# Performance work log

Measured on AMD Instinct MI355X. Metric: run time of the kernel, lower is better.

## Reference

```python
import jax, jax.numpy as jnp
import numpy as np

NUM_HEADS = 16
STRIDE = 32
WINDOW = 64  # local window half-width hard-coded in the original forward


def setup_inputs() -> dict:
    key = jax.random.key(0)
    k0, k1, k2 = jax.random.split(key, 3)
    d = 1024
    return {
        "x": jax.random.normal(k0, (1, 2048, d), dtype=jnp.float32),
        "w_qkv": jax.random.normal(k1, (d, 3 * d), dtype=jnp.float32) / np.sqrt(d),
        "b_qkv": jnp.zeros((3 * d,), dtype=jnp.float32),
        "w_out": jax.random.normal(k2, (d, d), dtype=jnp.float32) / np.sqrt(d),
        "b_out": jnp.zeros((d,), dtype=jnp.float32),
    }


def _sparse_mask(n: int) -> jnp.ndarray:
    # mask[i, j] True if j is a strided column (j % stride == 0)
    # or j is within the +/-WINDOW local band of i.
    i = jnp.arange(n)[:, None]
    j = jnp.arange(n)[None, :]
    return (j % STRIDE == 0) | (jnp.abs(i - j) <= WINDOW)


def reference(x, w_qkv, b_qkv, w_out, b_out):
    b, n, d = x.shape
    h = NUM_HEADS
    dh = d // h
    scale = dh ** (-0.5)

    qkv = x @ w_qkv + b_qkv  # [b, n, 3d]
    q, k, v = jnp.split(qkv, 3, axis=-1)
    q = q.reshape(b, n, h, dh).transpose(0, 2, 1, 3)  # [b, h, n, dh]
    k = k.reshape(b, n, h, dh).transpose(0, 2, 1, 3)
    v = v.reshape(b, n, h, dh).transpose(0, 2, 1, 3)

    scores = jnp.einsum("bhid,bhjd->bhij", q, k) * scale  # [b, h, n, n]
    mask = _sparse_mask(n)  # [n, n], broadcast over b, h
    scores = jnp.where(mask, scores, -jnp.inf)
    attn = jax.nn.softmax(scores, axis=-1)

    out = jnp.einsum("bhij,bhjd->bhid", attn, v)  # [b, h, n, dh]
    out = out.transpose(0, 2, 1, 3).reshape(b, n, d)
    return out @ w_out + b_out
```

## Files before the change

kernel.cpp:

```cpp
#include <hip/hip_runtime.h>

typedef unsigned short u16;
typedef __attribute__((ext_vector_type(8))) short bf16x8;
typedef __attribute__((ext_vector_type(4))) float f32x4;

__device__ __forceinline__ u16 f2bf(float f) {
  union { float f; unsigned u; } v; v.f = f;
  unsigned u = v.u;
  return (u16)((u + 0x7FFFu + ((u >> 16) & 1u)) >> 16);
}

__device__ __forceinline__ void gld16(const void* g, void* l) {
  __builtin_amdgcn_global_load_lds((const __attribute__((address_space(1))) void*)g,
                                   (__attribute__((address_space(3))) void*)l, 16, 0, 0);
}

__device__ __forceinline__ void tconv64(const float* __restrict__ in, u16* __restrict__ out,
                                        int R, int C, int bc, int br, float* t) {
  const int tid = threadIdx.x;
  const int c0 = bc * 64, r0 = br * 64;
  const int hi = tid >> 4, lo = tid & 15;
#pragma unroll
  for (int it = 0; it < 4; ++it) {
    int r = it * 16 + hi;
    float4 f = *(const float4*)&in[(size_t)(r0 + r) * C + c0 + lo * 4];
    float* tr = &t[r * 65 + lo * 4];
    tr[0] = f.x; tr[1] = f.y; tr[2] = f.z; tr[3] = f.w;
  }
  __syncthreads();
#pragma unroll
  for (int it = 0; it < 4; ++it) {
    int cc = it * 16 + hi;
    ushort4 o;
    o.x = f2bf(t[(lo * 4 + 0) * 65 + cc]);
    o.y = f2bf(t[(lo * 4 + 1) * 65 + cc]);
    o.z = f2bf(t[(lo * 4 + 2) * 65 + cc]);
    o.w = f2bf(t[(lo * 4 + 3) * 65 + cc]);
    *(ushort4*)&out[(size_t)(c0 + cc) * R + r0 + lo * 4] = o;
  }
}

__global__ __launch_bounds__(256) void prep(const float* __restrict__ x, u16* __restrict__ xb,
                                            const float* __restrict__ wq, u16* __restrict__ wqT,
                                            const float* __restrict__ wo, u16* __restrict__ woT) {
  __shared__ float t[64 * 65];
  int b = blockIdx.x;
  if (b < 1024) {
    int i = (b * 256 + threadIdx.x) * 8;
    float4 f0 = *(const float4*)(x + i);
    float4 f1 = *(const float4*)(x + i + 4);
    ushort4 r0, r1;
    r0.x = f2bf(f0.x); r0.y = f2bf(f0.y); r0.z = f2bf(f0.z); r0.w = f2bf(f0.w);
    r1.x = f2bf(f1.x); r1.y = f2bf(f1.y); r1.z = f2bf(f1.z); r1.w = f2bf(f1.w);
    *(ushort4*)(xb + i) = r0;
    *(ushort4*)(xb + i + 4) = r1;
  } else if (b < 1024 + 768) {
    int b2 = b - 1024;
    tconv64(wq, wqT, 1024, 3072, b2 % 48, b2 / 48, t);
  } else {
    int b3 = b - 1792;
    tconv64(wo, woT, 1024, 1024, b3 & 15, b3 >> 4, t);
  }
}

#define GEMM_STAGE(As, Bs, A, BT, buf, kt, BM, BN, MT, NT)                        \
  {                                                                               \
    _Pragma("unroll")                                                             \
    for (int it = 0; it < MT; ++it) {                                             \
      int G = wv * (MT * 64) + it * 64 + lane;                                    \
      int r = G >> 3, g = G & 7, gs = g ^ (r & 7);                                \
      gld16(&A[(size_t)(m0 + r) * K + (kt) + gs * 8],                             \
            &As[buf][(wv * (MT * 64) + it * 64) * 8]);                            \
    }                                                                             \
    _Pragma("unroll")                                                             \
    for (int it = 0; it < NT; ++it) {                                             \
      int G = wv * (NT * 64) + it * 64 + lane;                                    \
      int r = G >> 3, g = G & 7, gs = g ^ (r & 7);                                \
      gld16(&BT[(size_t)(n0 + r) * K + (kt) + gs * 8],                            \
            &Bs[buf][(wv * (NT * 64) + it * 64) * 8]);                            \
    }                                                                             \
  }

#define GEMM_COMPUTE(As, Bs, buf, BM, BN, MT, NT)                                 \
  {                                                                               \
    _Pragma("unroll")                                                             \
    for (int ks = 0; ks < 2; ++ks) {                                              \
      bf16x8 av[MT], bv[NT];                                                      \
      _Pragma("unroll")                                                           \
      for (int m = 0; m < MT; ++m) {                                              \
        int r = wm * (BM / 2) + m * 16 + lr;                                      \
        av[m] = *(const bf16x8*)&As[buf][r * 64 + (((ks * 4 + lg) ^ (r & 7)) * 8)]; \
      }                                                                           \
      _Pragma("unroll")                                                           \
      for (int n = 0; n < NT; ++n) {                                              \
        int r = wn * (BN / 2) + n * 16 + lr;                                      \
        bv[n] = *(const bf16x8*)&Bs[buf][r * 64 + (((ks * 4 + lg) ^ (r & 7)) * 8)]; \
      }                                                                           \
      _Pragma("unroll")                                                           \
      for (int m = 0; m < MT; ++m)                                                \
        _Pragma("unroll")                                                         \
        for (int n = 0; n < NT; ++n)                                              \
          acc[m][n] = __builtin_amdgcn_mfma_f32_16x16x32_bf16(av[m], bv[n],       \
                                                              acc[m][n], 0, 0, 0); \
    }                                                                             \
  }

__global__ __launch_bounds__(256) void gemm_qkv(const u16* __restrict__ A,
                                                const u16* __restrict__ BT,
                                                const float* __restrict__ bias,
                                                u16* __restrict__ qkv3,
                                                u16* __restrict__ vT,
                                                u16* __restrict__ vTs,
                                                int K) {
  constexpr int BM = 128, BN = 64, MT = 4, NT = 2;
  __shared__ u16 As[2][BM * 64];
  __shared__ u16 Bs[2][BN * 64];
  const int tid = threadIdx.x;
  const int lane = tid & 63, wv = tid >> 6;
  const int lr = lane & 15, lg = lane >> 4;
  const int wm = wv >> 1, wn = wv & 1;
  const int m0 = blockIdx.y * BM, n0 = blockIdx.x * BN;

  f32x4 acc[MT][NT] = {};

  GEMM_STAGE(As, Bs, A, BT, 0, 0, BM, BN, MT, NT);
  __syncthreads();
  int cur = 0;
  for (int kt = 64; kt < K; kt += 64) {
    GEMM_STAGE(As, Bs, A, BT, cur ^ 1, kt, BM, BN, MT, NT);
    GEMM_COMPUTE(As, Bs, cur, BM, BN, MT, NT);
    __syncthreads();
    cur ^= 1;
  }
  GEMM_COMPUTE(As, Bs, cur, BM, BN, MT, NT);

  if (n0 < 2048) {
#pragma unroll
    for (int m = 0; m < MT; ++m)
#pragma unroll
      for (int n = 0; n < NT; ++n) {
        int col = n0 + wn * 32 + n * 16 + lr;
        float bcol = bias[col];
#pragma unroll
        for (int qq = 0; qq < 4; ++qq) {
          int row = m0 + wm * 64 + m * 16 + 4 * lg + qq;
          qkv3[(size_t)row * 3072 + col] = f2bf(acc[m][n][qq] + bcol);
        }
      }
  } else {
    __syncthreads();
    u16* T = &As[0][0];
#pragma unroll
    for (int m = 0; m < MT; ++m)
#pragma unroll
      for (int n = 0; n < NT; ++n) {
        int col = wn * 32 + n * 16 + lr;
        float bcol = bias[n0 + col];
#pragma unroll
        for (int qq = 0; qq < 4; ++qq) {
          int row = wm * 64 + m * 16 + 4 * lg + qq;
          T[col * 132 + row] = f2bf(acc[m][n][qq] + bcol);
        }
      }
    __syncthreads();
    const int dgb = n0 - 2048;
#pragma unroll
    for (int c = wv; c < 64; c += 4) {
      uint val = (uint)T[c * 132 + lane * 2] | ((uint)T[c * 132 + lane * 2 + 1] << 16);
      *(uint*)&vT[(size_t)(dgb + c) * 2048 + m0 + lane * 2] = val;
    }
    {
      int rr = tid >> 6, c = tid & 63;
      vTs[(size_t)(dgb + c) * 64 + (m0 >> 5) + rr] = T[c * 132 + rr * 32];
    }
  }
}

__global__ __launch_bounds__(256) void gemm_out(const u16* __restrict__ A,
                                                const u16* __restrict__ BT,
                                                const float* __restrict__ bias,
                                                float* __restrict__ Cp,
                                                int K) {
  constexpr int BM = 64, BN = 64, MT = 2, NT = 2;
  __shared__ u16 As[2][BM * 64];
  __shared__ u16 Bs[2][BN * 64];
  const int tid = threadIdx.x;
  const int lane = tid & 63, wv = tid >> 6;
  const int lr = lane & 15, lg = lane >> 4;
  const int wm = wv >> 1, wn = wv & 1;
  const int m0 = blockIdx.y * BM, n0 = blockIdx.x * BN;

  f32x4 acc[MT][NT] = {};

  GEMM_STAGE(As, Bs, A, BT, 0, 0, BM, BN, MT, NT);
  __syncthreads();
  int cur = 0;
  for (int kt = 64; kt < K; kt += 64) {
    GEMM_STAGE(As, Bs, A, BT, cur ^ 1, kt, BM, BN, MT, NT);
    GEMM_COMPUTE(As, Bs, cur, BM, BN, MT, NT);
    __syncthreads();
    cur ^= 1;
  }
  GEMM_COMPUTE(As, Bs, cur, BM, BN, MT, NT);

#pragma unroll
  for (int m = 0; m < MT; ++m)
#pragma unroll
    for (int n = 0; n < NT; ++n) {
      int col = n0 + wn * 32 + n * 16 + lr;
      float bcol = bias[col];
#pragma unroll
      for (int qq = 0; qq < 4; ++qq) {
        int row = m0 + wm * 32 + m * 16 + 4 * lg + qq;
        Cp[(size_t)row * 1024 + col] = acc[m][n][qq] + bcol;
      }
    }
}

__global__ __launch_bounds__(64) void sattn(const u16* __restrict__ qkv,
                                            const u16* __restrict__ vT,
                                            const u16* __restrict__ vTs,
                                            u16* __restrict__ ao) {
  const int h = blockIdx.x;
  const int i0 = blockIdx.y * 16;
  const int ws = i0 - 64;
  const int lane = threadIdx.x;
  const int lr = lane & 15, lg = lane >> 4;

  __shared__ __attribute__((aligned(16))) u16 Ps[16][232];

  const u16* qp = &qkv[(size_t)(i0 + lr) * 3072 + h * 64 + lg * 8];
  bf16x8 qa0 = *(const bf16x8*)qp;
  bf16x8 qa1 = *(const bf16x8*)(qp + 32);

  const u16* kp[13];
#pragma unroll
  for (int n = 0; n < 13; ++n) {
    int col = n * 16 + lr;
    int j = (col < 144) ? (ws + col) : ((col - 144) << 5);
    j = j < 0 ? 0 : (j > 2047 ? 2047 : j);
    kp[n] = &qkv[(size_t)j * 3072 + 1024 + h * 64 + lg * 8];
  }

  f32x4 sc[13];
#pragma unroll
  for (int n = 0; n < 13; ++n) {
    bf16x8 k0 = *(const bf16x8*)kp[n];
    bf16x8 k1 = *(const bf16x8*)(kp[n] + 32);
    f32x4 a = {0.f, 0.f, 0.f, 0.f};
    a = __builtin_amdgcn_mfma_f32_16x16x32_bf16(qa0, k0, a, 0, 0, 0);
    a = __builtin_amdgcn_mfma_f32_16x16x32_bf16(qa1, k1, a, 0, 0, 0);
    sc[n] = a;
  }

  float mx[4] = {-1e30f, -1e30f, -1e30f, -1e30f};
#pragma unroll
  for (int n = 0; n < 13; ++n) {
    int col = n * 16 + lr;
    int jw = ws + col;
    int js = (col - 144) << 5;
    bool isw = col < 144;
#pragma unroll
    for (int qq = 0; qq < 4; ++qq) {
      int i = i0 + 4 * lg + qq;
      bool ok;
      if (isw) {
        int dd = i - jw; dd = dd < 0 ? -dd : dd;
        ok = (jw >= 0) && (jw < 2048) && ((dd <= 64) || ((jw & 31) == 0));
      } else {
        ok = (js < ws) || (js > ws + 143);
      }
      float v = ok ? sc[n][qq] * 0.125f : -1e30f;
      sc[n][qq] = v;
      mx[qq] = fmaxf(mx[qq], v);
    }
  }
#pragma unroll
  for (int qq = 0; qq < 4; ++qq) {
    float v = mx[qq];
    v = fmaxf(v, __shfl_xor(v, 1));
    v = fmaxf(v, __shfl_xor(v, 2));
    v = fmaxf(v, __shfl_xor(v, 4));
    v = fmaxf(v, __shfl_xor(v, 8));
    mx[qq] = v;
  }

  float sm[4] = {0.f, 0.f, 0.f, 0.f};
#pragma unroll
  for (int n = 0; n < 13; ++n) {
#pragma unroll
    for (int qq = 0; qq < 4; ++qq) {
      float p = __expf(sc[n][qq] - mx[qq]);
      sm[qq] += p;
      Ps[4 * lg + qq][n * 16 + lr] = f2bf(p);
    }
  }
#pragma unroll
  for (int qq = 0; qq < 4; ++qq) {
    float s = sm[qq];
    s += __shfl_xor(s, 1);
    s += __shfl_xor(s, 2);
    s += __shfl_xor(s, 4);
    s += __shfl_xor(s, 8);
    sm[qq] = s;
  }
  {
    ushort4 z; z.x = 0; z.y = 0; z.z = 0; z.w = 0;
    *(ushort4*)&Ps[lane >> 2][208 + (lane & 3) * 4] = z;
  }
  __syncthreads();

  f32x4 ov[4] = {{0.f,0.f,0.f,0.f},{0.f,0.f,0.f,0.f},{0.f,0.f,0.f,0.f},{0.f,0.f,0.f,0.f}};
#pragma unroll
  for (int ksb = 0; ksb < 7; ++ksb) {
    bf16x8 pa = *(const bf16x8*)&Ps[lr][ksb * 32 + lg * 8];
    int c0 = ksb * 32 + lg * 8;
#pragma unroll
    for (int n = 0; n < 4; ++n) {
      int d = n * 16 + lr;
      const u16* vp;
      if (c0 < 144) {
        int jb = ws + c0;
        jb = jb < 0 ? 0 : (jb > 2040 ? 2040 : jb);
        vp = &vT[(size_t)(h * 64 + d) * 2048 + jb];
      } else if (c0 < 208) {
        vp = &vTs[((size_t)(h * 64 + d) << 6) + (c0 - 144)];
      } else {
        vp = &vTs[(size_t)(h * 64 + d) << 6];
      }
      bf16x8 vb = *(const bf16x8*)vp;
      ov[n] = __builtin_amdgcn_mfma_f32_16x16x32_bf16(pa, vb, ov[n], 0, 0, 0);
    }
  }

#pragma unroll
  for (int qq = 0; qq < 4; ++qq) {
    float inv = 1.0f / sm[qq];
    int row = i0 + 4 * lg + qq;
#pragma unroll
    for (int n = 0; n < 4; ++n)
      ao[(size_t)row * 1024 + h * 64 + n * 16 + lr] = f2bf(ov[n][qq] * inv);
  }
}

extern "C" void kernel_launch(void* const* d_in, const int* in_sizes, int n_in,
                              void* d_out, int out_size, void* d_ws, size_t ws_size,
                              hipStream_t stream) {
  (void)in_sizes; (void)n_in; (void)out_size; (void)ws_size;
  const float* x     = (const float*)d_in[0];
  const float* w_qkv = (const float*)d_in[1];
  const float* b_qkv = (const float*)d_in[2];
  const float* w_out = (const float*)d_in[3];
  const float* b_out = (const float*)d_in[4];
  float* out = (float*)d_out;
  char* ws = (char*)d_ws;

  u16* xb    = (u16*)(ws);
  u16* wqkvT = (u16*)(ws + 4194304);
  u16* woutT = (u16*)(ws + 10485760);
  u16* qkv3  = (u16*)(ws + 12582912);
  u16* attnb = (u16*)(ws + 25165824);
  u16* vT    = (u16*)(ws + 29360128);
  u16* vTs   = (u16*)(ws + 33554432);

  prep<<<2048, 256, 0, stream>>>(x, xb, w_qkv, wqkvT, w_out, woutT);
  gemm_qkv<<<dim3(3072 / 64, 2048 / 128), 256, 0, stream>>>(xb, wqkvT, b_qkv, qkv3, vT, vTs,
                                                            1024);
  sattn<<<dim3(16, 128), 64, 0, stream>>>(qkv3, vT, vTs, attnb);
  gemm_out<<<dim3(1024 / 64, 2048 / 64), 256, 0, stream>>>(attnb, woutT, b_out, out, 1024);
}
```

Baseline: 63.14 us.

## Stage shared K/V tiles in LDS across four query waves per attention block

The sparse attention kernel now processes 64 query rows per block with four waves. Each block loads a 192-column window of K plus 64 strided columns, and the matching V^T slice, into swizzled LDS using direct global-to-LDS loads, so the waves share them instead of each wave fetching K/V from global memory on its own. The window widens from 144 to 192 columns, which adds masked MFMA work, and the larger LDS footprint may reduce occupancy.

```diff
diff --git a/kernel.cpp b/kernel.cpp
--- a/kernel.cpp
+++ b/kernel.cpp
@@ -217,36 +217,59 @@
     }
 }
 
-__global__ __launch_bounds__(64) void sattn(const u16* __restrict__ qkv,
-                                            const u16* __restrict__ vT,
-                                            const u16* __restrict__ vTs,
-                                            u16* __restrict__ ao) {
+__global__ __launch_bounds__(256) void sattn(const u16* __restrict__ qkv,
+                                             const u16* __restrict__ vT,
+                                             const u16* __restrict__ vTs,
+                                             u16* __restrict__ ao) {
   const int h = blockIdx.x;
-  const int i0 = blockIdx.y * 16;
-  const int ws = i0 - 64;
-  const int lane = threadIdx.x;
+  const int i0b = blockIdx.y * 64;
+  const int ws = i0b - 64;
+  const int tid = threadIdx.x;
+  const int lane = tid & 63, wv = tid >> 6;
   const int lr = lane & 15, lg = lane >> 4;
 
-  __shared__ __attribute__((aligned(16))) u16 Ps[16][232];
-
+  __shared__ __attribute__((aligned(16))) u16 Kl[256 * 64];
+  __shared__ __attribute__((aligned(16))) u16 Vl[64 * 256];
+  __shared__ __attribute__((aligned(16))) u16 Ps[4][16][264];
+
+#pragma unroll
+  for (int it = 0; it < 8; ++it) {
+    {
+      int ck = wv * 8 + it;
+      int c = 8 * ck + (lane >> 3);
+      int g = lane & 7, gs = g ^ (c & 7);
+      int j = (c < 192) ? (ws + c) : ((c - 192) << 5);
+      j = j < 0 ? 0 : (j > 2047 ? 2047 : j);
+      gld16(&qkv[(size_t)j * 3072 + 1024 + h * 64 + gs * 8], &Kl[ck * 512]);
+    }
+    {
+      int tv = wv * 8 + it;
+      int d = 2 * tv + (lane >> 5);
+      int g = lane & 31, gs = g ^ (d & 7);
+      const u16* src;
+      if (gs < 24) {
+        int c0 = ws + gs * 8;
+        c0 = c0 < 0 ? 0 : (c0 > 2040 ? 2040 : c0);
+        src = &vT[(size_t)(h * 64 + d) * 2048 + c0];
+      } else {
+        src = &vTs[(size_t)(h * 64 + d) * 64 + (gs - 24) * 8];
+      }
+      gld16(src, &Vl[tv * 512]);
+    }
+  }
+  __syncthreads();
+
+  const int i0 = i0b + wv * 16;
   const u16* qp = &qkv[(size_t)(i0 + lr) * 3072 + h * 64 + lg * 8];
   bf16x8 qa0 = *(const bf16x8*)qp;
   bf16x8 qa1 = *(const bf16x8*)(qp + 32);
 
-  const u16* kp[13];
-#pragma unroll
-  for (int n = 0; n < 13; ++n) {
-    int col = n * 16 + lr;
-    int j = (col < 144) ? (ws + col) : ((col - 144) << 5);
-    j = j < 0 ? 0 : (j > 2047 ? 2047 : j);
-    kp[n] = &qkv[(size_t)j * 3072 + 1024 + h * 64 + lg * 8];
-  }
-
-  f32x4 sc[13];
-#pragma unroll
-  for (int n = 0; n < 13; ++n) {
-    bf16x8 k0 = *(const bf16x8*)kp[n];
-    bf16x8 k1 = *(const bf16x8*)(kp[n] + 32);
+  f32x4 sc[16];
+#pragma unroll
+  for (int n = 0; n < 16; ++n) {
+    int c = n * 16 + lr;
+    bf16x8 k0 = *(const bf16x8*)&Kl[c * 64 + ((lg ^ (c & 7)) * 8)];
+    bf16x8 k1 = *(const bf16x8*)&Kl[c * 64 + (((4 + lg) ^ (c & 7)) * 8)];
     f32x4 a = {0.f, 0.f, 0.f, 0.f};
     a = __builtin_amdgcn_mfma_f32_16x16x32_bf16(qa0, k0, a, 0, 0, 0);
     a = __builtin_amdgcn_mfma_f32_16x16x32_bf16(qa1, k1, a, 0, 0, 0);
@@ -255,11 +278,11 @@
 
   float mx[4] = {-1e30f, -1e30f, -1e30f, -1e30f};
 #pragma unroll
-  for (int n = 0; n < 13; ++n) {
-    int col = n * 16 + lr;
-    int jw = ws + col;
-    int js = (col - 144) << 5;
-    bool isw = col < 144;
+  for (int n = 0; n < 16; ++n) {
+    int c = n * 16 + lr;
+    int jw = ws + c;
+    int js = (c - 192) << 5;
+    bool isw = c < 192;
 #pragma unroll
     for (int qq = 0; qq < 4; ++qq) {
       int i = i0 + 4 * lg + qq;
@@ -268,7 +291,7 @@
         int dd = i - jw; dd = dd < 0 ? -dd : dd;
         ok = (jw >= 0) && (jw < 2048) && ((dd <= 64) || ((jw & 31) == 0));
       } else {
-        ok = (js < ws) || (js > ws + 143);
+        ok = (js < ws) || (js >= ws + 192);
       }
       float v = ok ? sc[n][qq] * 0.125f : -1e30f;
       sc[n][qq] = v;
@@ -287,12 +310,12 @@
 
   float sm[4] = {0.f, 0.f, 0.f, 0.f};
 #pragma unroll
-  for (int n = 0; n < 13; ++n) {
+  for (int n = 0; n < 16; ++n) {
 #pragma unroll
     for (int qq = 0; qq < 4; ++qq) {
       float p = __expf(sc[n][qq] - mx[qq]);
       sm[qq] += p;
-      Ps[4 * lg + qq][n * 16 + lr] = f2bf(p);
+      Ps[wv][4 * lg + qq][n * 16 + lr] = f2bf(p);
     }
   }
 #pragma unroll
@@ -304,31 +327,16 @@
     s += __shfl_xor(s, 8);
     sm[qq] = s;
   }
-  {
-    ushort4 z; z.x = 0; z.y = 0; z.z = 0; z.w = 0;
-    *(ushort4*)&Ps[lane >> 2][208 + (lane & 3) * 4] = z;
-  }
   __syncthreads();
 
   f32x4 ov[4] = {{0.f,0.f,0.f,0.f},{0.f,0.f,0.f,0.f},{0.f,0.f,0.f,0.f},{0.f,0.f,0.f,0.f}};
 #pragma unroll
-  for (int ksb = 0; ksb < 7; ++ksb) {
-    bf16x8 pa = *(const bf16x8*)&Ps[lr][ksb * 32 + lg * 8];
-    int c0 = ksb * 32 + lg * 8;
+  for (int ksb = 0; ksb < 8; ++ksb) {
+    bf16x8 pa = *(const bf16x8*)&Ps[wv][lr][ksb * 32 + lg * 8];
 #pragma unroll
     for (int n = 0; n < 4; ++n) {
       int d = n * 16 + lr;
-      const u16* vp;
-      if (c0 < 144) {
-        int jb = ws + c0;
-        jb = jb < 0 ? 0 : (jb > 2040 ? 2040 : jb);
-        vp = &vT[(size_t)(h * 64 + d) * 2048 + jb];
-      } else if (c0 < 208) {
-        vp = &vTs[((size_t)(h * 64 + d) << 6) + (c0 - 144)];
-      } else {
-        vp = &vTs[(size_t)(h * 64 + d) << 6];
-      }
-      bf16x8 vb = *(const bf16x8*)vp;
+      bf16x8 vb = *(const bf16x8*)&Vl[d * 256 + (((ksb * 4 + lg) ^ (d & 7)) * 8)];
       ov[n] = __builtin_amdgcn_mfma_f32_16x16x32_bf16(pa, vb, ov[n], 0, 0, 0);
     }
   }
@@ -366,6 +374,6 @@
   prep<<<2048, 256, 0, stream>>>(x, xb, w_qkv, wqkvT, w_out, woutT);
   gemm_qkv<<<dim3(3072 / 64, 2048 / 128), 256, 0, stream>>>(xb, wqkvT, b_qkv, qkv3, vT, vTs,
                                                             1024);
-  sattn<<<dim3(16, 128), 64, 0, stream>>>(qkv3, vT, vTs, attnb);
+  sattn<<<dim3(16, 32), 256, 0, stream>>>(qkv3, vT, vTs, attnb);
   gemm_out<<<dim3(1024 / 64, 2048 / 64), 256, 0, stream>>>(attnb, woutT, b_out, out, 1024);
 }
```

New measurement: 59.51 us. 5.7% less time.
